# Kernel tuning notes

Measured on AMD Instinct MI355X. Metric: run time of the kernel, lower is better.

## Reference

```python
import jax, jax.numpy as jnp
import numpy as np

B, S, D = 4, 1024, 1024
H = 16
DH = D // H           # 64
ROT = 64              # rotary_emb_dim (full head dim)
NEG_INF = -10000.0
ROPE_BASE = 10000.0


def _rope_tables(seqlen, rot_dim, dtype=jnp.float32):
    inv_freq = 1.0 / (ROPE_BASE ** (jnp.arange(0, rot_dim, 2, dtype=jnp.float32) / rot_dim))
    t = jnp.arange(seqlen, dtype=jnp.float32)
    freqs = jnp.einsum('s,f->sf', t, inv_freq)  # (S, rot_dim//2)
    return jnp.cos(freqs).astype(dtype), jnp.sin(freqs).astype(dtype)


def _apply_rotary(x, cos, sin):
    # x: (B, S, H, DH); GPT-NeoX (non-interleaved) rotary over first ROT dims
    half = ROT // 2
    x_rot, x_pass = x[..., :ROT], x[..., ROT:]
    x1, x2 = x_rot[..., :half], x_rot[..., half:]
    c = cos[None, :, None, :]
    s = sin[None, :, None, :]
    rot = jnp.concatenate([x1 * c - x2 * s, x2 * c + x1 * s], axis=-1)
    return jnp.concatenate([rot, x_pass], axis=-1) if x_pass.shape[-1] else rot


def setup_inputs() -> dict:
    key = jax.random.key(0)
    ks = jax.random.split(key, 5)
    sc_in = 1.0 / np.sqrt(D)
    return {
        'x': jax.random.normal(ks[0], (B, S, D), jnp.float32),
        'Wqkv': jax.random.normal(ks[1], (3 * D, D), jnp.float32) * sc_in,
        'bqkv': jax.random.normal(ks[2], (3 * D,), jnp.float32) * 0.01,
        'Wout': jax.random.normal(ks[3], (D, D), jnp.float32) * sc_in,
        'bout': jax.random.normal(ks[4], (D,), jnp.float32) * 0.01,
    }


def reference(x, Wqkv, bqkv, Wout, bout):
    # QKV projection: (B,S,D) -> (B,S,3,H,DH)
    qkv = (jnp.einsum('bsd,ed->bse', x, Wqkv) + bqkv).reshape(B, S, 3, H, DH)
    q, k, v = qkv[:, :, 0], qkv[:, :, 1], qkv[:, :, 2]
    cos, sin = _rope_tables(S, ROT, q.dtype)
    q = _apply_rotary(q, cos, sin)
    k = _apply_rotary(k, cos, sin)
    scale = 1.0 / np.sqrt(DH)
    scores = jnp.einsum('bthd,bshd->bhts', q, k * scale)  # (B,H,S,S)
    causal_mask = jnp.triu(jnp.full((S, S), NEG_INF, dtype=scores.dtype), 1)
    scores = scores + causal_mask
    attn = jax.nn.softmax(scores, axis=-1)
    out = jnp.einsum('bhts,bshd->bthd', attn, v).reshape(B, S, D)
    return jnp.einsum('bsd,ed->bse', out, Wout) + bout
```

## Files before the change

kernel.cpp:

```cpp
#include <hip/hip_runtime.h>

#define B_ 4
#define S_ 1024
#define D_ 1024
#define H_ 16
#define DH_ 64

typedef unsigned short u16;
typedef __attribute__((ext_vector_type(8))) short bf16x8;
typedef __attribute__((ext_vector_type(4))) float f32x4;

__device__ __forceinline__ float bf2f(u16 h){
  union { unsigned u; float f; } x; x.u = ((unsigned)h) << 16; return x.f;
}
__device__ __forceinline__ u16 f2bf(float f){
  union { float f; unsigned u; } x; x.f = f;
  unsigned u = x.u;
  return (u16)((u + 0x7fffu + ((u >> 16) & 1u)) >> 16);
}

__device__ __forceinline__ void gload16(const u16* g, u16* l){
  __builtin_amdgcn_global_load_lds(
      (const __attribute__((address_space(1))) unsigned int*)g,
      (__attribute__((address_space(3))) unsigned int*)l, 16, 0, 0);
}

__global__ __launch_bounds__(256) void cast3tab(
    const float* __restrict__ a, u16* __restrict__ oa, int na,
    const float* __restrict__ b, u16* __restrict__ ob, int nb,
    const float* __restrict__ c, u16* __restrict__ oc,
    float2* __restrict__ tab){
  if (blockIdx.x >= 8192){
    int idx = (blockIdx.x - 8192) * 256 + threadIdx.x;
    int s = idx >> 5, i = idx & 31;
    float invf = powf(10000.0f, -(float)i * (1.0f / 32.0f));
    float sn, cs;
    sincosf((float)s * invf, &sn, &cs);
    tab[idx] = make_float2(cs, sn);
    return;
  }
  int i = (blockIdx.x * 256 + threadIdx.x) * 4;
  const float* src; u16* dst;
  if (i < na){ src = a + i; dst = oa + i; }
  else if (i < na + nb){ src = b + (i - na); dst = ob + (i - na); }
  else { src = c + (i - na - nb); dst = oc + (i - na - nb); }
  float4 v = *(const float4*)src;
  union { u16 s[4]; uint2 u; } o;
  o.s[0] = f2bf(v.x); o.s[1] = f2bf(v.y); o.s[2] = f2bf(v.z); o.s[3] = f2bf(v.w);
  *(uint2*)dst = o.u;
}

__global__ __launch_bounds__(256, 3) void gemm_qkv(const u16* __restrict__ A,
    const u16* __restrict__ Bm, const float* __restrict__ bias,
    const float2* __restrict__ tab,
    u16* __restrict__ qb, u16* __restrict__ kb, u16* __restrict__ vtb){
  __shared__ u16 As_[2][128*32];
  __shared__ u16 Bs_[2][128*32];
  const int K = 1024;
  const int tid = threadIdx.x;
  const int lane = tid & 63, w = tid >> 6;
  const int wr = w >> 1, wc = w & 1;
  const int lo = lane & 15, g = lane >> 4;

  const int bid = blockIdx.x;
  const int swz = (bid & 7) * 96 + (bid >> 3);
  const int mx = swz & 31, ny = swz >> 5;
  const int m0 = mx * 128, n0 = ny * 128;

  f32x4 acc[4][4];
  #pragma unroll
  for (int i = 0; i < 4; ++i)
    #pragma unroll
    for (int j = 0; j < 4; ++j) acc[i][j] = (f32x4){0.f, 0.f, 0.f, 0.f};

  auto stage = [&](int b, int kt){
    const u16* ga = A + (size_t)m0 * K + kt * 32;
    const u16* gb = Bm + (size_t)n0 * K + kt * 32;
    #pragma unroll
    for (int it = 0; it < 2; ++it){
      int c = tid + it * 256;
      int r = c >> 2;
      int cbs = ((c & 3) * 16) ^ ((r & 3) << 4);
      gload16(ga + r * K + (cbs >> 1), &As_[b][c * 8]);
      gload16(gb + r * K + (cbs >> 1), &Bs_[b][c * 8]);
    }
  };

  auto rdA = [&](int b, int fm) -> bf16x8 {
    int row = wr*64 + fm*16 + lo;
    int byte = row*64 + ((g*16) ^ ((row & 3) << 4));
    return *(const bf16x8*)(&As_[b][byte >> 1]);
  };
  auto rdB = [&](int b, int fn) -> bf16x8 {
    int row = wc*64 + fn*16 + lo;
    int byte = row*64 + ((g*16) ^ ((row & 3) << 4));
    return *(const bf16x8*)(&Bs_[b][byte >> 1]);
  };

  auto ktile = [&](int b, int stage_t){
    bf16x8 af[4], bf[4];
    #pragma unroll
    for (int fm = 0; fm < 4; ++fm) af[fm] = rdA(b, fm);
    #pragma unroll
    for (int fn = 0; fn < 4; ++fn) bf[fn] = rdB(b, fn);
    asm volatile("s_waitcnt lgkmcnt(0)" ::: "memory");
    __builtin_amdgcn_sched_barrier(0);
    __builtin_amdgcn_s_setprio(1);
    #pragma unroll
    for (int fm = 0; fm < 4; ++fm)
      #pragma unroll
      for (int fn = 0; fn < 2; ++fn)
        acc[fm][fn] = __builtin_amdgcn_mfma_f32_16x16x32_bf16(af[fm], bf[fn], acc[fm][fn], 0, 0, 0);
    __builtin_amdgcn_s_setprio(0);
    __builtin_amdgcn_s_barrier();
    if (stage_t >= 0) stage(b, stage_t);
    __builtin_amdgcn_s_setprio(1);
    #pragma unroll
    for (int fm = 0; fm < 4; ++fm)
      #pragma unroll
      for (int fn = 2; fn < 4; ++fn)
        acc[fm][fn] = __builtin_amdgcn_mfma_f32_16x16x32_bf16(af[fm], bf[fn], acc[fm][fn], 0, 0, 0);
    __builtin_amdgcn_s_setprio(0);
  };

  stage(0, 0);
  stage(1, 1);
  for (int t = 0; t < 30; ++t){
    asm volatile("s_waitcnt vmcnt(4)" ::: "memory");
    __builtin_amdgcn_s_barrier();
    __builtin_amdgcn_sched_barrier(0);
    ktile(t & 1, t + 2);
  }
  asm volatile("s_waitcnt vmcnt(4)" ::: "memory");
  __builtin_amdgcn_s_barrier();
  __builtin_amdgcn_sched_barrier(0);
  ktile(0, -1);
  asm volatile("s_waitcnt vmcnt(0)" ::: "memory");
  __builtin_amdgcn_s_barrier();
  __builtin_amdgcn_sched_barrier(0);
  ktile(1, -1);

  const int gcb = n0 + wc*64;
  const int ty = gcb >> 10;
  const int h  = (gcb >> 6) & 15;
  float bv[4];
  #pragma unroll
  for (int fn = 0; fn < 4; ++fn) bv[fn] = bias[gcb + fn*16 + lo - wc*64 + wc*64];
  #pragma unroll
  for (int fn = 0; fn < 4; ++fn) bv[fn] = bias[gcb + fn*16 + lo];

  if (ty < 2){
    u16* dst = (ty == 0) ? qb : kb;
    #pragma unroll
    for (int fm = 0; fm < 4; ++fm){
      #pragma unroll
      for (int j = 0; j < 4; ++j){
        int row = m0 + wr*64 + fm*16 + g*4 + j;
        int bb = row >> 10, s = row & 1023;
        size_t obase = (((size_t)(bb * H_ + h)) * S_ + s) * DH_;
        #pragma unroll
        for (int fn = 0; fn < 2; ++fn){
          int i = fn*16 + lo;
          float2 t2 = tab[s*32 + i];
          float v1 = acc[fm][fn][j] + bv[fn];
          float v2 = acc[fm][fn+2][j] + bv[fn+2];
          dst[obase + i]      = f2bf(v1 * t2.x - v2 * t2.y);
          dst[obase + i + 32] = f2bf(v2 * t2.x + v1 * t2.y);
        }
      }
    }
  } else {
    __syncthreads();
    u16* wbase = (w < 2) ? ((u16*)As_ + w * 4096) : ((u16*)Bs_ + (w - 2) * 4096);
    #pragma unroll
    for (int fm = 0; fm < 4; ++fm)
      #pragma unroll
      for (int fn = 0; fn < 4; ++fn){
        int d = fn*16 + lo;
        #pragma unroll
        for (int j = 0; j < 4; ++j){
          int sl = fm*16 + g*4 + j;
          wbase[d*64 + (sl ^ ((d & 7) << 3))] = f2bf(acc[fm][fn][j] + bv[fn]);
        }
      }
    const int rowblk = m0 + wr*64;
    const int bb = rowblk >> 10;
    const int sbase = rowblk & 1023;
    #pragma unroll
    for (int pass = 0; pass < 16; ++pass){
      int d = pass*4 + g;
      int sc = lo * 4;
      uint2 v = *(const uint2*)(&wbase[d*64 + (sc ^ ((d & 7) << 3))]);
      *(uint2*)(vtb + (((size_t)(bb * H_ + h)) * DH_ + d) * S_ + sbase + sc) = v;
    }
  }
}

__global__ __launch_bounds__(256, 3) void gemm_out(const u16* __restrict__ A,
    const u16* __restrict__ Bm, const float* __restrict__ bias,
    float* __restrict__ Cout){
  __shared__ u16 As_[2][128*32];
  __shared__ u16 Bs_[2][128*32];
  const int K = 1024;
  const int tid = threadIdx.x;
  const int lane = tid & 63, w = tid >> 6;
  const int wr = w >> 1, wc = w & 1;
  const int lo = lane & 15, g = lane >> 4;

  const int bid = blockIdx.x;
  const int swz = (bid & 7) * 32 + (bid >> 3);
  const int mx = swz & 31, ny = swz >> 5;
  const int m0 = mx * 128, n0 = ny * 128;

  f32x4 acc[4][4];
  #pragma unroll
  for (int i = 0; i < 4; ++i)
    #pragma unroll
    for (int j = 0; j < 4; ++j) acc[i][j] = (f32x4){0.f, 0.f, 0.f, 0.f};

  auto stage = [&](int b, int kt){
    const u16* ga = A + (size_t)m0 * K + kt * 32;
    const u16* gb = Bm + (size_t)n0 * K + kt * 32;
    #pragma unroll
    for (int it = 0; it < 2; ++it){
      int c = tid + it * 256;
      int r = c >> 2;
      int cbs = ((c & 3) * 16) ^ ((r & 3) << 4);
      gload16(ga + r * K + (cbs >> 1), &As_[b][c * 8]);
      gload16(gb + r * K + (cbs >> 1), &Bs_[b][c * 8]);
    }
  };

  auto rdA = [&](int b, int fm) -> bf16x8 {
    int row = wr*64 + fm*16 + lo;
    int byte = row*64 + ((g*16) ^ ((row & 3) << 4));
    return *(const bf16x8*)(&As_[b][byte >> 1]);
  };
  auto rdB = [&](int b, int fn) -> bf16x8 {
    int row = wc*64 + fn*16 + lo;
    int byte = row*64 + ((g*16) ^ ((row & 3) << 4));
    return *(const bf16x8*)(&Bs_[b][byte >> 1]);
  };

  auto ktile = [&](int b, int stage_t){
    bf16x8 af[4], bf[4];
    #pragma unroll
    for (int fm = 0; fm < 4; ++fm) af[fm] = rdA(b, fm);
    #pragma unroll
    for (int fn = 0; fn < 4; ++fn) bf[fn] = rdB(b, fn);
    asm volatile("s_waitcnt lgkmcnt(0)" ::: "memory");
    __builtin_amdgcn_sched_barrier(0);
    __builtin_amdgcn_s_setprio(1);
    #pragma unroll
    for (int fm = 0; fm < 4; ++fm)
      #pragma unroll
      for (int fn = 0; fn < 2; ++fn)
        acc[fm][fn] = __builtin_amdgcn_mfma_f32_16x16x32_bf16(af[fm], bf[fn], acc[fm][fn], 0, 0, 0);
    __builtin_amdgcn_s_setprio(0);
    __builtin_amdgcn_s_barrier();
    if (stage_t >= 0) stage(b, stage_t);
    __builtin_amdgcn_s_setprio(1);
    #pragma unroll
    for (int fm = 0; fm < 4; ++fm)
      #pragma unroll
      for (int fn = 2; fn < 4; ++fn)
        acc[fm][fn] = __builtin_amdgcn_mfma_f32_16x16x32_bf16(af[fm], bf[fn], acc[fm][fn], 0, 0, 0);
    __builtin_amdgcn_s_setprio(0);
  };

  stage(0, 0);
  stage(1, 1);
  for (int t = 0; t < 30; ++t){
    asm volatile("s_waitcnt vmcnt(4)" ::: "memory");
    __builtin_amdgcn_s_barrier();
    __builtin_amdgcn_sched_barrier(0);
    ktile(t & 1, t + 2);
  }
  asm volatile("s_waitcnt vmcnt(4)" ::: "memory");
  __builtin_amdgcn_s_barrier();
  __builtin_amdgcn_sched_barrier(0);
  ktile(0, -1);
  asm volatile("s_waitcnt vmcnt(0)" ::: "memory");
  __builtin_amdgcn_s_barrier();
  __builtin_amdgcn_sched_barrier(0);
  ktile(1, -1);

  #pragma unroll
  for (int fm = 0; fm < 4; ++fm){
    #pragma unroll
    for (int j = 0; j < 4; ++j){
      int row = m0 + wr*64 + fm*16 + g*4 + j;
      #pragma unroll
      for (int fn = 0; fn < 4; ++fn){
        int col = n0 + wc*64 + fn*16 + lo;
        Cout[(size_t)row * 1024 + col] = acc[fm][fn][j] + bias[col];
      }
    }
  }
}

__global__ __launch_bounds__(256) void attn_fwd(const u16* __restrict__ qb,
    const u16* __restrict__ kb, const u16* __restrict__ vtb,
    u16* __restrict__ ctx){
  const int bh = blockIdx.x;
  const int qt = 15 - blockIdx.y;
  const int b = bh >> 4, h = bh & 15;
  const int tid = threadIdx.x;
  const int lane = tid & 63, w = tid >> 6;
  const int lo = lane & 15, g = lane >> 4;

  __shared__ u16 Kl[2][64*64];
  __shared__ u16 Vl[2][64*64];
  __shared__ u16 Plds[4][16][64];

  auto stage = [&](int buf, int kt){
    const u16* ksrc = kb  + ((size_t)bh * S_ + kt*64) * DH_;
    const u16* vsrc = vtb + (size_t)bh * DH_ * S_ + kt*64;
    #pragma unroll
    for (int it = 0; it < 2; ++it){
      int c = tid + it * 256;
      int row = c >> 3;
      int colbs = ((c & 7) * 16) ^ ((row & 7) << 4);
      gload16(ksrc + (size_t)row * DH_ + (colbs >> 1), &Kl[buf][c * 8]);
      gload16(vsrc + (size_t)row * S_  + (colbs >> 1), &Vl[buf][c * 8]);
    }
  };

  stage(0, 0);

  bf16x8 qf[2];
  {
    const u16* qa = qb + ((size_t)bh * S_ + qt*64 + w*16 + lo) * DH_ + g*8;
    qf[0] = *(const bf16x8*)(qa);  qf[1] = *(const bf16x8*)(qa + 32);
  }

  float m_run[4], l_run[4];
  f32x4 O[4];
  #pragma unroll
  for (int j = 0; j < 4; ++j){ m_run[j] = -1e30f; l_run[j] = 0.f; }
  #pragma unroll
  for (int c = 0; c < 4; ++c) O[c] = (f32x4){0.f,0.f,0.f,0.f};

  int buf = 0;

  auto computeTile = [&](bool diag){
    f32x4 sacc[4];
    #pragma unroll
    for (int c = 0; c < 4; ++c) sacc[c] = (f32x4){0.f,0.f,0.f,0.f};
    __builtin_amdgcn_s_setprio(1);
    #pragma unroll
    for (int cf = 0; cf < 4; ++cf){
      int r = cf*16 + lo;
      #pragma unroll
      for (int ks = 0; ks < 2; ++ks){
        int byteoff = r*128 + ((ks*64 + g*16) ^ ((lo & 7) << 4));
        bf16x8 kf = *(const bf16x8*)(&Kl[buf][byteoff >> 1]);
        sacc[cf] = __builtin_amdgcn_mfma_f32_16x16x32_bf16(qf[ks], kf, sacc[cf], 0, 0, 0);
      }
    }
    __builtin_amdgcn_s_setprio(0);
    #pragma unroll
    for (int cf = 0; cf < 4; ++cf){
      #pragma unroll
      for (int j = 0; j < 4; ++j){
        float sv = sacc[cf][j] * 0.125f;
        if (diag){
          int kj = cf*16 + lo;
          int qr = w*16 + g*4 + j;
          if (kj > qr) sv -= 10000.f;
        }
        sacc[cf][j] = sv;
      }
    }
    float rowmax[4];
    #pragma unroll
    for (int j = 0; j < 4; ++j){
      float v = fmaxf(fmaxf(sacc[0][j], sacc[1][j]), fmaxf(sacc[2][j], sacc[3][j]));
      v = fmaxf(v, __shfl_xor(v, 1));
      v = fmaxf(v, __shfl_xor(v, 2));
      v = fmaxf(v, __shfl_xor(v, 4));
      v = fmaxf(v, __shfl_xor(v, 8));
      rowmax[j] = v;
    }
    float need = fmaxf(fmaxf(rowmax[0]-m_run[0], rowmax[1]-m_run[1]),
                       fmaxf(rowmax[2]-m_run[2], rowmax[3]-m_run[3]));
    float rsum[4] = {0.f,0.f,0.f,0.f};
    if (__all(need <= 8.0f)){
      #pragma unroll
      for (int cf = 0; cf < 4; ++cf)
        #pragma unroll
        for (int j = 0; j < 4; ++j){
          float pv = __expf(sacc[cf][j] - m_run[j]);
          sacc[cf][j] = pv;
          rsum[j] += pv;
        }
      #pragma unroll
      for (int j = 0; j < 4; ++j){
        float v = rsum[j];
        v += __shfl_xor(v, 1);
        v += __shfl_xor(v, 2);
        v += __shfl_xor(v, 4);
        v += __shfl_xor(v, 8);
        l_run[j] += v;
      }
    } else {
      float alpha[4];
      #pragma unroll
      for (int j = 0; j < 4; ++j){
        float mnew = fmaxf(m_run[j], rowmax[j]);
        alpha[j] = __expf(m_run[j] - mnew);
        m_run[j] = mnew;
      }
      #pragma unroll
      for (int cf = 0; cf < 4; ++cf)
        #pragma unroll
        for (int j = 0; j < 4; ++j){
          float pv = __expf(sacc[cf][j] - m_run[j]);
          sacc[cf][j] = pv;
          rsum[j] += pv;
        }
      #pragma unroll
      for (int j = 0; j < 4; ++j){
        float v = rsum[j];
        v += __shfl_xor(v, 1);
        v += __shfl_xor(v, 2);
        v += __shfl_xor(v, 4);
        v += __shfl_xor(v, 8);
        l_run[j] = l_run[j] * alpha[j] + v;
      }
      #pragma unroll
      for (int c = 0; c < 4; ++c)
        #pragma unroll
        for (int j = 0; j < 4; ++j) O[c][j] *= alpha[j];
    }

    #pragma unroll
    for (int cf = 0; cf < 4; ++cf){
      #pragma unroll
      for (int jp = 0; jp < 2; ++jp){
        unsigned pk;
        asm("v_cvt_pk_bf16_f32 %0, %1, %2"
            : "=v"(pk) : "v"(sacc[cf][jp*2]), "v"(sacc[cf][jp*2+1]));
        int r1 = g*4 + jp*2, r2 = r1 + 1;
        Plds[w][r1][(cf*16 + lo) ^ ((r1 & 7) << 3)] = (u16)(pk & 0xffffu);
        Plds[w][r2][(cf*16 + lo) ^ ((r2 & 7) << 3)] = (u16)(pk >> 16);
      }
    }

    __builtin_amdgcn_s_setprio(1);
    #pragma unroll
    for (int ks = 0; ks < 2; ++ks){
      bf16x8 pf = *(const bf16x8*)(&Plds[w][lo][(ks*32 + g*8) ^ ((lo & 7) << 3)]);
      #pragma unroll
      for (int ocf = 0; ocf < 4; ++ocf){
        int r = ocf*16 + lo;
        int byteoff = r*128 + ((ks*64 + g*16) ^ ((lo & 7) << 4));
        bf16x8 vf = *(const bf16x8*)(&Vl[buf][byteoff >> 1]);
        O[ocf] = __builtin_amdgcn_mfma_f32_16x16x32_bf16(pf, vf, O[ocf], 0, 0, 0);
      }
    }
    __builtin_amdgcn_s_setprio(0);
  };

  for (int kt = 0; kt <= qt; ++kt){
    __syncthreads();
    if (kt < qt) stage(buf ^ 1, kt + 1);
    computeTile(kt == qt);
    buf ^= 1;
  }

  float inv[4];
  #pragma unroll
  for (int j = 0; j < 4; ++j) inv[j] = 1.0f / l_run[j];
  #pragma unroll
  for (int ocf = 0; ocf < 4; ++ocf){
    #pragma unroll
    for (int j = 0; j < 4; ++j){
      int d = ocf*16 + lo;
      int qi = qt*64 + w*16 + g*4 + j;
      ctx[((size_t)(b * S_ + qi)) * D_ + h * DH_ + d] = f2bf(O[ocf][j] * inv[j]);
    }
  }
}

extern "C" void kernel_launch(void* const* d_in, const int* in_sizes, int n_in,
                              void* d_out, int out_size, void* d_ws, size_t ws_size,
                              hipStream_t stream){
  (void)in_sizes; (void)n_in; (void)out_size; (void)ws_size;
  const float* x    = (const float*)d_in[0];
  const float* Wqkv = (const float*)d_in[1];
  const float* bqkv = (const float*)d_in[2];
  const float* Wout = (const float*)d_in[3];
  const float* bout = (const float*)d_in[4];
  float* out = (float*)d_out;

  char* p = (char*)d_ws;
  u16* x_bf    = (u16*)p; p += (size_t)4096*1024*2;
  u16* wqkv_bf = (u16*)p; p += (size_t)3072*1024*2;
  u16* wout_bf = (u16*)p; p += (size_t)1024*1024*2;
  u16* q_bf    = (u16*)p; p += (size_t)4096*1024*2;
  u16* k_bf    = (u16*)p; p += (size_t)4096*1024*2;
  u16* vt_bf   = (u16*)p; p += (size_t)4096*1024*2;
  u16* ctx_bf  = (u16*)p; p += (size_t)4096*1024*2;
  float2* tab  = (float2*)p; p += (size_t)1024*32*8;

  const int na = 4096*1024, nb = 3072*1024;
  cast3tab<<<8320, 256, 0, stream>>>(x, x_bf, na, Wqkv, wqkv_bf, nb, Wout, wout_bf, tab);

  gemm_qkv<<<768, 256, 0, stream>>>(x_bf, wqkv_bf, bqkv, tab, q_bf, k_bf, vt_bf);

  attn_fwd<<<dim3(64, 16), 256, 0, stream>>>(q_bf, k_bf, vt_bf, ctx_bf);

  gemm_out<<<256, 256, 0, stream>>>(ctx_bf, wout_bf, bout, out);
}
```

Before: 102.1 us.

## Load K/V fragments directly from global memory in attention, dropping LDS staging

The attention kernel no longer stages K and V tiles into double-buffered shared memory through async global-to-LDS loads and a per-tile barrier. Each wave now reads its K and V MFMA fragments straight from global memory into registers every key tile. This removes the block barrier and the LDS traffic, and lowers LDS use, which may raise occupancy. In exchange each of the four waves fetches the same K/V data separately, raising L2/global traffic, and load latency is no longer overlapped by prefetching the next tile. A duplicated bias load in the QKV epilogue is also removed.

```diff
diff --git a/kernel.cpp b/kernel.cpp
--- a/kernel.cpp
+++ b/kernel.cpp
@@ -145,8 +145,6 @@
   const int h  = (gcb >> 6) & 15;
   float bv[4];
   #pragma unroll
-  for (int fn = 0; fn < 4; ++fn) bv[fn] = bias[gcb + fn*16 + lo - wc*64 + wc*64];
-  #pragma unroll
   for (int fn = 0; fn < 4; ++fn) bv[fn] = bias[gcb + fn*16 + lo];
 
   if (ty < 2){
@@ -309,24 +307,7 @@
   const int lane = tid & 63, w = tid >> 6;
   const int lo = lane & 15, g = lane >> 4;
 
-  __shared__ u16 Kl[2][64*64];
-  __shared__ u16 Vl[2][64*64];
   __shared__ u16 Plds[4][16][64];
-
-  auto stage = [&](int buf, int kt){
-    const u16* ksrc = kb  + ((size_t)bh * S_ + kt*64) * DH_;
-    const u16* vsrc = vtb + (size_t)bh * DH_ * S_ + kt*64;
-    #pragma unroll
-    for (int it = 0; it < 2; ++it){
-      int c = tid + it * 256;
-      int row = c >> 3;
-      int colbs = ((c & 7) * 16) ^ ((row & 7) << 4);
-      gload16(ksrc + (size_t)row * DH_ + (colbs >> 1), &Kl[buf][c * 8]);
-      gload16(vsrc + (size_t)row * S_  + (colbs >> 1), &Vl[buf][c * 8]);
-    }
-  };
-
-  stage(0, 0);
 
   bf16x8 qf[2];
   {
@@ -341,24 +322,37 @@
   #pragma unroll
   for (int c = 0; c < 4; ++c) O[c] = (f32x4){0.f,0.f,0.f,0.f};
 
-  int buf = 0;
-
-  auto computeTile = [&](bool diag){
+  const u16* kbh = kb  + (size_t)bh * S_ * DH_;
+  const u16* vbh = vtb + (size_t)bh * DH_ * S_;
+
+  for (int kt = 0; kt <= qt; ++kt){
+    const bool diag = (kt == qt);
+    const u16* kbase = kbh + (size_t)kt * 64 * DH_;
+    const u16* vbase = vbh + kt * 64;
+
+    bf16x8 kf[8], vf[8];
+    #pragma unroll
+    for (int cf = 0; cf < 4; ++cf)
+      #pragma unroll
+      for (int ks = 0; ks < 2; ++ks)
+        kf[cf*2+ks] = *(const bf16x8*)(kbase + (cf*16 + lo)*DH_ + ks*32 + g*8);
+    #pragma unroll
+    for (int ocf = 0; ocf < 4; ++ocf)
+      #pragma unroll
+      for (int ks = 0; ks < 2; ++ks)
+        vf[ocf*2+ks] = *(const bf16x8*)(vbase + (size_t)(ocf*16 + lo)*S_ + ks*32 + g*8);
+
     f32x4 sacc[4];
     #pragma unroll
     for (int c = 0; c < 4; ++c) sacc[c] = (f32x4){0.f,0.f,0.f,0.f};
     __builtin_amdgcn_s_setprio(1);
     #pragma unroll
-    for (int cf = 0; cf < 4; ++cf){
-      int r = cf*16 + lo;
-      #pragma unroll
-      for (int ks = 0; ks < 2; ++ks){
-        int byteoff = r*128 + ((ks*64 + g*16) ^ ((lo & 7) << 4));
-        bf16x8 kf = *(const bf16x8*)(&Kl[buf][byteoff >> 1]);
-        sacc[cf] = __builtin_amdgcn_mfma_f32_16x16x32_bf16(qf[ks], kf, sacc[cf], 0, 0, 0);
-      }
-    }
-    __builtin_amdgcn_s_setprio(0);
+    for (int cf = 0; cf < 4; ++cf)
+      #pragma unroll
+      for (int ks = 0; ks < 2; ++ks)
+        sacc[cf] = __builtin_amdgcn_mfma_f32_16x16x32_bf16(qf[ks], kf[cf*2+ks], sacc[cf], 0, 0, 0);
+    __builtin_amdgcn_s_setprio(0);
+
     #pragma unroll
     for (int cf = 0; cf < 4; ++cf){
       #pragma unroll
@@ -452,21 +446,10 @@
     for (int ks = 0; ks < 2; ++ks){
       bf16x8 pf = *(const bf16x8*)(&Plds[w][lo][(ks*32 + g*8) ^ ((lo & 7) << 3)]);
       #pragma unroll
-      for (int ocf = 0; ocf < 4; ++ocf){
-        int r = ocf*16 + lo;
-        int byteoff = r*128 + ((ks*64 + g*16) ^ ((lo & 7) << 4));
-        bf16x8 vf = *(const bf16x8*)(&Vl[buf][byteoff >> 1]);
-        O[ocf] = __builtin_amdgcn_mfma_f32_16x16x32_bf16(pf, vf, O[ocf], 0, 0, 0);
-      }
-    }
-    __builtin_amdgcn_s_setprio(0);
-  };
-
-  for (int kt = 0; kt <= qt; ++kt){
-    __syncthreads();
-    if (kt < qt) stage(buf ^ 1, kt + 1);
-    computeTile(kt == qt);
-    buf ^= 1;
+      for (int ocf = 0; ocf < 4; ++ocf)
+        O[ocf] = __builtin_amdgcn_mfma_f32_16x16x32_bf16(pf, vf[ocf*2+ks], O[ocf], 0, 0, 0);
+    }
+    __builtin_amdgcn_s_setprio(0);
   }
 
   float inv[4];
```

After: 132.3 us. 1.3x slower.
